# Kernel tuning notes

Measured on AMD Instinct MI355X. Metric: run time of the kernel, lower is better.

The kernel has to match this reference:

```python
import jax, jax.numpy as jnp
import numpy as np

NOISE_SCALE = 1.0  # GumbelDistribution(0.0, noise_scale)
INPUT_NOISE_TEMP = 1.0
EPS = 1e-10


def setup_inputs() -> dict:
    key = jax.random.key(0)
    k1, k2 = jax.random.split(key)
    S, B, N = 16, 128, 16384
    logits = jax.random.normal(k1, (B, N), dtype=jnp.float32)
    uniform_noise = jax.random.uniform(k2, (S, B, N), dtype=jnp.float32,
                                       minval=EPS, maxval=1.0 - EPS)
    return {"logits": logits, "uniform_noise": uniform_noise, "k": 32}


def _topk_mask(perturbed, k):
    # select_from_candidates: hard 0/1 mask of the top-k candidates per row.
    S, B, N = perturbed.shape
    flat = perturbed.reshape(S * B, N)
    _, idx = jax.lax.top_k(flat, k)                      # [S*B, k]
    rows = jnp.arange(S * B)[:, None]
    mask = jnp.zeros_like(flat).at[rows, idx].set(1.0)
    return mask.reshape(S, B, N)


def reference(logits, uniform_noise, k):
    # IMLE forward: replicate logits nb_samples times, add Gumbel noise,
    # then top-k hard selection per sample.
    gumbel = -jnp.log(-jnp.log(uniform_noise)) * NOISE_SCALE  # Gumbel(0, scale)
    perturbed = logits[None, :, :] + INPUT_NOISE_TEMP * gumbel  # [S, B, N]
    mask = _topk_mask(perturbed, k)
    return mask
```

## Files before the change

### kernel.cpp

```cpp
#include <hip/hip_runtime.h>
#include <math.h>

typedef unsigned int uint32;
typedef unsigned long long uint64;

#define NN      16384
#define THREADS 256
#define VPT     16
#define NCOPY   16
#define EQ_CAP  256

__device__ __forceinline__ float cr_logf(float x)
{
    const uint32 xb = __float_as_uint(x);
    const uint32 ge = (xb >> 22) & 1u;
    const int    e  = (int)(xb >> 23) - 127 + (int)ge;
    const uint32 mb = (xb & 0x7FFFFFu) | 0x3F800000u;
    const float  mh = __uint_as_float(mb - (ge << 23));
    const double md  = (double)mh;
    const double num = md - 1.0;
    const double den = md + 1.0;
    double r = (double)__builtin_amdgcn_rcpf((float)den);
    r = r * fma(-den, r, 2.0);
    r = r * fma(-den, r, 2.0);
    const double s  = num * r;
    const double s2 = s * s;
    double q;
    q = 1.0/23.0;
    q = fma(q, s2, 1.0/21.0);
    q = fma(q, s2, 1.0/19.0);
    q = fma(q, s2, 1.0/17.0);
    q = fma(q, s2, 1.0/15.0);
    q = fma(q, s2, 1.0/13.0);
    q = fma(q, s2, 1.0/11.0);
    q = fma(q, s2, 1.0/9.0);
    q = fma(q, s2, 1.0/7.0);
    q = fma(q, s2, 1.0/5.0);
    q = fma(q, s2, 1.0/3.0);
    const double s3 = s2 * (2.0 * s);
    const double lm = fma(s3, q, 2.0 * s);
    const double ed = (double)e;
    const double LN2_HI = 6.93147180369123816490e-01;
    const double LN2_LO = 1.90821492927058770002e-10;
    return (float)fma(ed, LN2_HI, fma(ed, LN2_LO, lm));
}

__global__ __launch_bounds__(THREADS, 4)
void imle_topk_kernel(const float* __restrict__ logits,
                      const float* __restrict__ noise,
                      const int*   __restrict__ kptr,
                      float*       __restrict__ out,
                      int Brows)
{
    __shared__ int     hist[256 * NCOPY];
    __shared__ int     finalh[256];
    __shared__ uint32  sh_pref;
    __shared__ int     sh_rem;
    __shared__ int     eq_cnt;
    __shared__ int     eq_idx[EQ_CAP];

    const int row  = blockIdx.x;
    const int lrow = row % Brows;
    const int tid  = threadIdx.x;
    const int k    = kptr[0];
    const int lane = tid & 63;
    const int wid  = tid >> 6;

    if (tid == 0) eq_cnt = 0;

    const float4* __restrict__ np4 = (const float4*)(noise  + (size_t)row  * NN);
    const float4* __restrict__ lp4 = (const float4*)(logits + (size_t)lrow * NN);
    float4*       __restrict__ op4 = (float4*)(out + (size_t)row * NN);

    uint32 key[VPT][4];

    #pragma unroll
    for (int j = 0; j < VPT; ++j) {
        const int v = tid + j * THREADS;
        const float4 u4 = np4[v];
        const float4 l4 = lp4[v];
        const float uu[4] = {u4.x, u4.y, u4.z, u4.w};
        const float ll[4] = {l4.x, l4.y, l4.z, l4.w};
        #pragma unroll
        for (int c = 0; c < 4; ++c) {
            const float t1 = cr_logf(uu[c]);
            const float t2 = cr_logf(-t1);
            const float p  = ll[c] - t2;
            const uint32 b = __float_as_uint(p);
            key[j][c] = (b & 0x80000000u) ? ~b : (b | 0x80000000u);
        }
    }

    __syncthreads();

    uint32 prefix = 0, himask = 0;
    int    rem    = k;
    const int copy = tid & (NCOPY - 1);

    #pragma unroll
    for (int dgt = 3; dgt >= 0; --dgt) {
        const int sh = 8 * dgt;

        #pragma unroll
        for (int i = 0; i < (256 * NCOPY) / THREADS; ++i)
            hist[tid + i * THREADS] = 0;
        __syncthreads();

        #pragma unroll
        for (int j = 0; j < VPT; ++j) {
            #pragma unroll
            for (int c = 0; c < 4; ++c) {
                const uint32 kk = key[j][c];
                if ((kk & himask) == prefix)
                    atomicAdd(&hist[(((kk >> sh) & 255u) * NCOPY) + copy], 1);
            }
        }
        __syncthreads();

        {
            int ssum = 0;
            #pragma unroll
            for (int q = 0; q < NCOPY; ++q)
                ssum += hist[tid * NCOPY + ((q + tid) & (NCOPY - 1))];
            finalh[tid] = ssum;
        }
        __syncthreads();

        if (wid == 0) {
            const int lo = 252 - 4 * lane;
            const int s  = finalh[lo] + finalh[lo+1] + finalh[lo+2] + finalh[lo+3];
            int p = s;
            #pragma unroll
            for (int off = 1; off < 64; off <<= 1) {
                const int v = __shfl_up(p, off);
                if (lane >= off) p += v;
            }
            const uint64 bal = __ballot(p >= rem);
            const int l0 = __ffsll((long long)bal) - 1;
            if (lane == l0) {
                int acc = p - s;
                int b   = lo + 3;
                for (;;) {
                    const int h = finalh[b];
                    if (acc + h >= rem || b == lo) break;
                    acc += h; --b;
                }
                sh_pref = prefix | ((uint32)b << sh);
                sh_rem  = rem - acc;
            }
        }
        __syncthreads();
        prefix = sh_pref;
        rem    = sh_rem;
        himask |= (0xFFu << sh);
    }

    const uint32 T     = prefix;
    const int    tneed = rem;

    #pragma unroll
    for (int j = 0; j < VPT; ++j) {
        const int v = tid + j * THREADS;
        float o[4];
        #pragma unroll
        for (int c = 0; c < 4; ++c) {
            const uint32 kk = key[j][c];
            o[c] = (kk > T) ? 1.0f : 0.0f;
            if (kk == T) {
                const int slot = atomicAdd(&eq_cnt, 1);
                if (slot < EQ_CAP) eq_idx[slot] = 4 * v + c;
            }
        }
        op4[v] = make_float4(o[0], o[1], o[2], o[3]);
    }
    __syncthreads();

    if (tid == 0) {
        int e = eq_cnt; if (e > EQ_CAP) e = EQ_CAP;
        float* orow = out + (size_t)row * NN;
        for (int it = 0; it < tneed; ++it) {
            int mn = 0x7FFFFFFF, mpos = -1;
            for (int q = 0; q < e; ++q) {
                const int idx = eq_idx[q];
                if (idx >= 0 && idx < mn) { mn = idx; mpos = q; }
            }
            if (mpos < 0) break;
            eq_idx[mpos] = -1;
            orow[mn] = 1.0f;
        }
    }
}

extern "C" void kernel_launch(void* const* d_in, const int* in_sizes, int n_in,
                              void* d_out, int out_size, void* d_ws, size_t ws_size,
                              hipStream_t stream) {
    const float* logits = (const float*)d_in[0];
    const float* noise  = (const float*)d_in[1];
    const int*   kptr   = (const int*)d_in[2];
    float*       out    = (float*)d_out;

    const int rows  = in_sizes[1] / NN;
    const int Brows = in_sizes[0] / NN;

    imle_topk_kernel<<<rows, THREADS, 0, stream>>>(logits, noise, kptr, out, Brows);
}
```

Baseline: 279.1 us.

## Use fast approximate logs with exact recompute on a small candidate set

Replaces the double-precision correctly-rounded log on every element with hardware log2-based float approximations, plus a short series near u=1. The radix select now runs only two byte passes to get an approximate threshold. Every element above a slightly lowered margin becomes a candidate, gets its key recomputed with the exact log, and is ranked against the others. The output is zero-filled early and ones are scattered afterwards. This removes most of the double-precision math and two histogram passes, but risks wrong results if the margin or the candidate cap is exceeded.

```diff
diff --git a/kernel.cpp b/kernel.cpp
--- a/kernel.cpp
+++ b/kernel.cpp
@@ -4,11 +4,20 @@
 typedef unsigned int uint32;
 typedef unsigned long long uint64;
 
-#define NN      16384
-#define THREADS 256
-#define VPT     16
-#define NCOPY   16
-#define EQ_CAP  256
+#define NN       16384
+#define THREADS  256
+#define VPT      16
+#define NCOPY    16
+#define CAND_CAP 1024
+
+__device__ __forceinline__ uint32 fkey(float p) {
+    const uint32 b = __float_as_uint(p);
+    return (b & 0x80000000u) ? ~b : (b | 0x80000000u);
+}
+__device__ __forceinline__ float fkey_dec(uint32 kk) {
+    const uint32 b = (kk & 0x80000000u) ? (kk ^ 0x80000000u) : ~kk;
+    return __uint_as_float(b);
+}
 
 __device__ __forceinline__ float cr_logf(float x)
 {
@@ -45,6 +54,35 @@
     return (float)fma(ed, LN2_HI, fma(ed, LN2_LO, lm));
 }
 
+__device__ __forceinline__ void select_byte(const int* __restrict__ finalh,
+                                            int rem_in, uint32* sh_bin,
+                                            int* sh_rem, int lane, int wid)
+{
+    if (wid == 0) {
+        const int lo = 252 - 4 * lane;
+        const int s  = finalh[lo] + finalh[lo+1] + finalh[lo+2] + finalh[lo+3];
+        int p = s;
+        #pragma unroll
+        for (int off = 1; off < 64; off <<= 1) {
+            const int v = __shfl_up(p, off);
+            if (lane >= off) p += v;
+        }
+        const uint64 bal = __ballot(p >= rem_in);
+        const int l0 = __ffsll((long long)bal) - 1;
+        if (lane == l0) {
+            int acc = p - s;
+            int b   = lo + 3;
+            for (;;) {
+                const int h = finalh[b];
+                if (acc + h >= rem_in || b == lo) break;
+                acc += h; --b;
+            }
+            *sh_bin = (uint32)b;
+            *sh_rem = rem_in - acc;
+        }
+    }
+}
+
 __global__ __launch_bounds__(THREADS, 4)
 void imle_topk_kernel(const float* __restrict__ logits,
                       const float* __restrict__ noise,
@@ -52,12 +90,13 @@
                       float*       __restrict__ out,
                       int Brows)
 {
-    __shared__ int     hist[256 * NCOPY];
-    __shared__ int     finalh[256];
-    __shared__ uint32  sh_pref;
-    __shared__ int     sh_rem;
-    __shared__ int     eq_cnt;
-    __shared__ int     eq_idx[EQ_CAP];
+    __shared__ int    hist[256 * NCOPY];
+    __shared__ int    finalh[256];
+    __shared__ uint32 sh_bin;
+    __shared__ int    sh_rem;
+    __shared__ int    cand_cnt;
+    __shared__ int    cand_idx[CAND_CAP];
+    __shared__ uint32 cand_key[CAND_CAP];
 
     const int row  = blockIdx.x;
     const int lrow = row % Brows;
@@ -66,13 +105,14 @@
     const int lane = tid & 63;
     const int wid  = tid >> 6;
 
-    if (tid == 0) eq_cnt = 0;
+    if (tid == 0) cand_cnt = 0;
 
     const float4* __restrict__ np4 = (const float4*)(noise  + (size_t)row  * NN);
     const float4* __restrict__ lp4 = (const float4*)(logits + (size_t)lrow * NN);
     float4*       __restrict__ op4 = (float4*)(out + (size_t)row * NN);
 
     uint32 key[VPT][4];
+    const float4 zero4 = make_float4(0.f, 0.f, 0.f, 0.f);
 
     #pragma unroll
     for (int j = 0; j < VPT; ++j) {
@@ -83,111 +123,110 @@
         const float ll[4] = {l4.x, l4.y, l4.z, l4.w};
         #pragma unroll
         for (int c = 0; c < 4; ++c) {
-            const float t1 = cr_logf(uu[c]);
-            const float t2 = cr_logf(-t1);
+            const float u  = uu[c];
+            const float d  = u - 1.0f;
+            const float t1g = __log2f(u) * 0.69314718056f;
+            const float t1w = d * fmaf(d, fmaf(d, fmaf(d, -0.25f, 0.33333334f), -0.5f), 1.0f);
+            const float t1 = (fabsf(d) < 0.015625f) ? t1w : t1g;
+            const float t2 = __log2f(-t1) * 0.69314718056f;
             const float p  = ll[c] - t2;
-            const uint32 b = __float_as_uint(p);
-            key[j][c] = (b & 0x80000000u) ? ~b : (b | 0x80000000u);
-        }
-    }
-
-    __syncthreads();
-
-    uint32 prefix = 0, himask = 0;
-    int    rem    = k;
+            key[j][c] = fkey(p);
+        }
+        op4[v] = zero4;
+    }
+    __syncthreads();
+
     const int copy = tid & (NCOPY - 1);
-
-    #pragma unroll
-    for (int dgt = 3; dgt >= 0; --dgt) {
-        const int sh = 8 * dgt;
-
-        #pragma unroll
-        for (int i = 0; i < (256 * NCOPY) / THREADS; ++i)
-            hist[tid + i * THREADS] = 0;
-        __syncthreads();
-
-        #pragma unroll
-        for (int j = 0; j < VPT; ++j) {
-            #pragma unroll
-            for (int c = 0; c < 4; ++c) {
-                const uint32 kk = key[j][c];
-                if ((kk & himask) == prefix)
-                    atomicAdd(&hist[(((kk >> sh) & 255u) * NCOPY) + copy], 1);
-            }
-        }
-        __syncthreads();
-
-        {
-            int ssum = 0;
-            #pragma unroll
-            for (int q = 0; q < NCOPY; ++q)
-                ssum += hist[tid * NCOPY + ((q + tid) & (NCOPY - 1))];
-            finalh[tid] = ssum;
-        }
-        __syncthreads();
-
-        if (wid == 0) {
-            const int lo = 252 - 4 * lane;
-            const int s  = finalh[lo] + finalh[lo+1] + finalh[lo+2] + finalh[lo+3];
-            int p = s;
-            #pragma unroll
-            for (int off = 1; off < 64; off <<= 1) {
-                const int v = __shfl_up(p, off);
-                if (lane >= off) p += v;
-            }
-            const uint64 bal = __ballot(p >= rem);
-            const int l0 = __ffsll((long long)bal) - 1;
-            if (lane == l0) {
-                int acc = p - s;
-                int b   = lo + 3;
-                for (;;) {
-                    const int h = finalh[b];
-                    if (acc + h >= rem || b == lo) break;
-                    acc += h; --b;
-                }
-                sh_pref = prefix | ((uint32)b << sh);
-                sh_rem  = rem - acc;
-            }
-        }
-        __syncthreads();
-        prefix = sh_pref;
-        rem    = sh_rem;
-        himask |= (0xFFu << sh);
-    }
-
-    const uint32 T     = prefix;
-    const int    tneed = rem;
-
-    #pragma unroll
-    for (int j = 0; j < VPT; ++j) {
-        const int v = tid + j * THREADS;
-        float o[4];
+    #pragma unroll
+    for (int i = 0; i < (256 * NCOPY) / THREADS; ++i)
+        hist[tid + i * THREADS] = 0;
+    __syncthreads();
+    #pragma unroll
+    for (int j = 0; j < VPT; ++j) {
+        #pragma unroll
+        for (int c = 0; c < 4; ++c)
+            atomicAdd(&hist[((key[j][c] >> 24) * NCOPY) + copy], 1);
+    }
+    __syncthreads();
+    {
+        int ssum = 0;
+        #pragma unroll
+        for (int q = 0; q < NCOPY; ++q)
+            ssum += hist[tid * NCOPY + ((q + tid) & (NCOPY - 1))];
+        finalh[tid] = ssum;
+    }
+    __syncthreads();
+    select_byte(finalh, k, &sh_bin, &sh_rem, lane, wid);
+    __syncthreads();
+    const uint32 b3  = sh_bin;
+    const int    rem = sh_rem;
+
+    __syncthreads();
+    #pragma unroll
+    for (int i = 0; i < (256 * NCOPY) / THREADS; ++i)
+        hist[tid + i * THREADS] = 0;
+    __syncthreads();
+    #pragma unroll
+    for (int j = 0; j < VPT; ++j) {
         #pragma unroll
         for (int c = 0; c < 4; ++c) {
             const uint32 kk = key[j][c];
-            o[c] = (kk > T) ? 1.0f : 0.0f;
-            if (kk == T) {
-                const int slot = atomicAdd(&eq_cnt, 1);
-                if (slot < EQ_CAP) eq_idx[slot] = 4 * v + c;
+            if ((kk >> 24) == b3)
+                atomicAdd(&hist[(((kk >> 16) & 255u) * NCOPY) + copy], 1);
+        }
+    }
+    __syncthreads();
+    {
+        int ssum = 0;
+        #pragma unroll
+        for (int q = 0; q < NCOPY; ++q)
+            ssum += hist[tid * NCOPY + ((q + tid) & (NCOPY - 1))];
+        finalh[tid] = ssum;
+    }
+    __syncthreads();
+    select_byte(finalh, rem, &sh_bin, &sh_rem, lane, wid);
+    __syncthreads();
+    const uint32 b2 = sh_bin;
+
+    const uint32 Lkey  = (b3 << 24) | (b2 << 16);
+    const float  Lf    = fkey_dec(Lkey);
+    const float  TloF  = Lf - (3e-4f + fabsf(Lf) * 2e-6f);
+    const uint32 Tlo   = fkey(TloF);
+
+    #pragma unroll
+    for (int j = 0; j < VPT; ++j) {
+        const int v = tid + j * THREADS;
+        #pragma unroll
+        for (int c = 0; c < 4; ++c) {
+            if (key[j][c] >= Tlo) {
+                const int slot = atomicAdd(&cand_cnt, 1);
+                if (slot < CAND_CAP) cand_idx[slot] = 4 * v + c;
             }
         }
-        op4[v] = make_float4(o[0], o[1], o[2], o[3]);
-    }
-    __syncthreads();
-
-    if (tid == 0) {
-        int e = eq_cnt; if (e > EQ_CAP) e = EQ_CAP;
-        float* orow = out + (size_t)row * NN;
-        for (int it = 0; it < tneed; ++it) {
-            int mn = 0x7FFFFFFF, mpos = -1;
-            for (int q = 0; q < e; ++q) {
-                const int idx = eq_idx[q];
-                if (idx >= 0 && idx < mn) { mn = idx; mpos = q; }
-            }
-            if (mpos < 0) break;
-            eq_idx[mpos] = -1;
-            orow[mn] = 1.0f;
-        }
+    }
+    __syncthreads();
+    int n = cand_cnt; if (n > CAND_CAP) n = CAND_CAP;
+
+    const float* __restrict__ nrow = noise  + (size_t)row  * NN;
+    const float* __restrict__ lrp  = logits + (size_t)lrow * NN;
+    for (int t = tid; t < n; t += THREADS) {
+        const int   idx = cand_idx[t];
+        const float t1  = cr_logf(nrow[idx]);
+        const float t2  = cr_logf(-t1);
+        cand_key[t] = fkey(lrp[idx] - t2);
+    }
+    __syncthreads();
+
+    float* __restrict__ orow = out + (size_t)row * NN;
+    for (int t = tid; t < n; t += THREADS) {
+        const uint32 mk = cand_key[t];
+        const int    mi = cand_idx[t];
+        int rank = 0;
+        for (int j2 = 0; j2 < n; ++j2) {
+            const uint32 ok = cand_key[j2];
+            rank += (ok > mk || (ok == mk && cand_idx[j2] < mi)) ? 1 : 0;
+        }
+        if (rank < k) orow[mi] = 1.0f;
     }
 }
 
```

Measured after the change: 259.3 us. -7.1%, faster.
